# Optimization experiments

Hardware: AMD Instinct MI355X
Metric: run time of the kernel (lower is better)

The kernel has to match this reference:

```python
import jax, jax.numpy as jnp
import numpy as np

SEQ, BATCH, IN_DIM, H1, H2, H3, OUT = 512, 4096, 4, 24, 48, 24, 2


def _rnn_layer(x, W_ih, W_hh, b_ih, b_hh):
    # x: [T, B, in]; torch RNN-relu cell: h_t = relu(x_t W_ih^T + b_ih + h_{t-1} W_hh^T + b_hh)
    pre = jnp.einsum('tbi,hi->tbh', x, W_ih) + (b_ih + b_hh)  # precompute input projection for all t

    def step(h, p):
        h = jax.nn.relu(p + h @ W_hh.T)
        return h, h

    h0 = jnp.zeros((x.shape[1], W_hh.shape[0]), x.dtype)
    _, ys = jax.lax.scan(step, h0, pre)
    return ys  # [T, B, hidden]


def setup_inputs() -> dict:
    key = jax.random.key(0)
    ks = jax.random.split(key, 14)

    def u(k, shape, fan):
        s = 1.0 / np.sqrt(fan)
        return jax.random.uniform(k, shape, jnp.float32, -s, s)

    return {
        'x': jax.random.normal(ks[0], (SEQ, BATCH, IN_DIM), jnp.float32),
        'W_ih0': u(ks[1], (H1, IN_DIM), H1), 'W_hh0': u(ks[2], (H1, H1), H1),
        'b_ih0': u(ks[3], (H1,), H1), 'b_hh0': u(ks[4], (H1,), H1),
        'W_ih1': u(ks[5], (H2, H1), H2), 'W_hh1': u(ks[6], (H2, H2), H2),
        'b_ih1': u(ks[7], (H2,), H2), 'b_hh1': u(ks[8], (H2,), H2),
        'W_ih2': u(ks[9], (H3, H2), H3), 'W_hh2': u(ks[10], (H3, H3), H3),
        'b_ih2': u(ks[11], (H3,), H3), 'b_hh2': u(ks[12], (H3,), H3),
        'W_out': u(ks[13], (OUT, H3), H3),
        'b_out': jnp.zeros((OUT,), jnp.float32),
    }


def reference(x, W_ih0, W_hh0, b_ih0, b_hh0, W_ih1, W_hh1, b_ih1, b_hh1,
              W_ih2, W_hh2, b_ih2, b_hh2, W_out, b_out):
    a1 = _rnn_layer(x, W_ih0, W_hh0, b_ih0, b_hh0)   # [T,B,24]
    a2 = _rnn_layer(a1, W_ih1, W_hh1, b_ih1, b_hh1)  # [T,B,48]
    a3 = _rnn_layer(a2, W_ih2, W_hh2, b_ih2, b_hh2)  # [T,B,24]
    return a3 @ W_out.T + b_out                       # [T,B,2]
```

## Files before the change

kernel.cpp:

```cpp
#include <hip/hip_runtime.h>
#include <hip/hip_fp16.h>


#define TSEQ 512
#define NBAT 4096

typedef float    f32x4 __attribute__((ext_vector_type(4)));
typedef _Float16 f16x8 __attribute__((ext_vector_type(8)));

union BFrag { f16x8 h; unsigned u[4]; };

__device__ __forceinline__ f32x4 MF(f16x8 a, f16x8 b, f32x4 c) {
  return __builtin_amdgcn_mfma_f32_16x16x32_f16(a, b, c, 0, 0, 0);
}
__device__ __forceinline__ unsigned pkh(float a, float b) {
  union { __half2 h2; unsigned u; } x;
  x.h2 = __floats2half2_rn(a, b);
  return x.u;
}
__device__ __forceinline__ unsigned pkr(float a, float b) {
  return pkh(fmaxf(a, 0.f), fmaxf(b, 0.f));
}

#define SBAR __builtin_amdgcn_sched_barrier(0)
#define LGKM_WAIT(n) __builtin_amdgcn_s_waitcnt(0xC07F | ((n) << 8))
#define ENDBAR(R)                                                              \
  do {                                                                         \
    SBAR;                                                                      \
    LGKM_WAIT(R);                                                              \
    __builtin_amdgcn_s_barrier();                                              \
    SBAR;                                                                      \
  } while (0)

#define SW16(PB, U) ((4 * (PB) + (U)) & 15)
#define SR16(PB, U) ((4 * (PB) + (U) + 12) & 15)

struct WP { const float *wih0,*whh0,*wih1,*whh1,*wih2,*whh2,*wout; };

__device__ float wcat(int layer, int m, int k, const WP& P) {
  if (layer == 0) {
    if (m < 24) {
      if (k < 24) return P.whh0[m * 24 + k];
      if (k >= 28 && k < 32) return P.wih0[m * 4 + (k - 28)];
    }
    return 0.f;
  } else if (layer == 1) {
    if (m < 48) {
      if (k < 24) return P.wih1[m * 24 + k];
      if (k >= 32 && k < 80) return P.whh1[m * 48 + (k - 32)];
    }
    return 0.f;
  } else if (layer == 2) {
    if (m < 24) {
      if (k < 48) return P.wih2[m * 48 + k];
      if (k >= 64 && k < 88) return P.whh2[m * 24 + (k - 64)];
    }
    return 0.f;
  } else {
    if (m < 2 && k < 24) return P.wout[m * 24 + k];
    return 0.f;
  }
}

__device__ f16x8 afrag(int layer, int mt, int kc, const WP& P) {
  int m  = mt * 16 + (threadIdx.x & 15);
  int kb = kc * 32 + 4 * ((threadIdx.x >> 4) & 3);
  f16x8 r;
#pragma unroll
  for (int j = 0; j < 4; ++j) r[j] = (_Float16)wcat(layer, m, kb + j, P);
#pragma unroll
  for (int j = 0; j < 4; ++j) r[4 + j] = (_Float16)wcat(layer, m, kb + 16 + j, P);
  return r;
}

__device__ f32x4 cfrag(const float* b1, const float* b2, int mt, int nvalid) {
  int qq = (threadIdx.x >> 4) & 3;
  f32x4 r;
#pragma unroll
  for (int i = 0; i < 4; ++i) {
    int m = mt * 16 + 4 * qq + i;
    float v = 0.f;
    if (m < nvalid) { v = b1[m]; if (b2) v += b2[m]; }
    r[i] = v;
  }
  return r;
}

__global__ void __launch_bounds__(512)
rnn3_p8s4(const float* __restrict__ x,
          const float* __restrict__ wih0, const float* __restrict__ whh0,
          const float* __restrict__ bih0, const float* __restrict__ bhh0,
          const float* __restrict__ wih1, const float* __restrict__ whh1,
          const float* __restrict__ bih1, const float* __restrict__ bhh1,
          const float* __restrict__ wih2, const float* __restrict__ whh2,
          const float* __restrict__ bih2, const float* __restrict__ bhh2,
          const float* __restrict__ wout, const float* __restrict__ bout,
          float* __restrict__ out) {
  __shared__ uint4 sH1[16][64];
  __shared__ f32x4 sP1[16][3][64];
  __shared__ uint4 sH2a[16][64];
  __shared__ uint2 sH2b[16][64];
  __shared__ f32x4 sP2a[16][64];
  __shared__ f32x4 sP2b[16][64];
  __shared__ uint4 sH3[16][64];

  const int tid  = threadIdx.x;
  const int wid  = tid >> 6;
  const int lane = tid & 63;
  const int c = lane & 15;
  const int q = lane >> 4;
  const int b0 = blockIdx.x * 16;

  WP P{wih0, whh0, wih1, whh1, wih2, whh2, wout};
  const float4* x4 = (const float4*)x;
  float2*       o2 = (float2*)out;

  const int NJ = 35;

  if (wid == 0) {
    f16x8 A00 = afrag(0, 0, 0, P), A01 = afrag(0, 1, 0, P);
    f32x4 C00 = cfrag(bih0, bhh0, 0, 24), C01 = cfrag(bih0, bhh0, 1, 24);
    float4 xb[16];
#pragma unroll
    for (int s = 0; s < 16; ++s) xb[s] = x4[(size_t)s * NBAT + b0 + c];
    unsigned fa0 = 0u, fa1 = 0u, fa2 = 0u, fa3 = 0u;

#define A_STEP(PB, U)                                                          \
    {                                                                          \
      float4 xs = xb[SW16(PB, U)];                                             \
      BFrag FAu;                                                               \
      FAu.u[0] = fa0; FAu.u[1] = fa1;                                          \
      FAu.u[2] = (q == 3) ? pkh(xs.x, xs.y) : fa2;                             \
      FAu.u[3] = (q == 3) ? pkh(xs.z, xs.w) : fa3;                             \
      f32x4 a10 = MF(A00, FAu.h, C00);                                         \
      f32x4 a11 = MF(A01, FAu.h, C01);                                         \
      {                                                                        \
        int t = 4 * i + (U);                                                   \
        int tn = (t + 16 < TSEQ) ? t + 16 : TSEQ - 1;                          \
        xb[SW16(PB, U)] = x4[(size_t)tn * NBAT + b0 + c];                      \
      }                                                                        \
      fa0 = pkr(a10[0], a10[1]); fa1 = pkr(a10[2], a10[3]);                    \
      fa2 = pkr(a11[0], a11[1]); fa3 = pkr(a11[2], a11[3]);                    \
      sH1[SW16(PB, U)][lane] = make_uint4(fa0, fa1, fa2, fa3);                 \
    }
#define A_BODY(PB)                                                             \
    {                                                                          \
      int i = i0 + (PB);                                                       \
      if (i <= 127) { A_STEP(PB, 0) A_STEP(PB, 1) A_STEP(PB, 2) A_STEP(PB, 3) }\
      ENDBAR(0);                                                               \
    }
#pragma unroll 1
    for (int J = 0; J < NJ; ++J) {
      int i0 = 4 * J;
      A_BODY(0) A_BODY(1) A_BODY(2) A_BODY(3)
    }
#undef A_BODY
#undef A_STEP

  } else if (wid == 1 || wid == 2) {
    const bool isD = (wid == 1);
    f16x8 W0 = afrag(1, isD ? 0 : 2, 0, P);
    f16x8 W1 = isD ? afrag(1, 1, 0, P) : W0;
    f32x4 Cb0 = cfrag(bih1, bhh1, isD ? 0 : 2, 48);
    f32x4 Cb1 = isD ? cfrag(bih1, bhh1, 1, 48) : Cb0;
    uint4 bufA[4], bufB[4];
#pragma unroll
    for (int s = 0; s < 4; ++s) { bufA[s] = make_uint4(0u,0u,0u,0u); bufB[s] = make_uint4(0u,0u,0u,0u); }

#define D_STEP(PB, U, CUR)                                                     \
    {                                                                          \
      BFrag FAu;                                                               \
      FAu.u[0] = CUR[U].x; FAu.u[1] = CUR[U].y;                                \
      FAu.u[2] = CUR[U].z; FAu.u[3] = CUR[U].w;                                \
      f32x4 p0 = MF(W0, FAu.h, Cb0);                                           \
      if (isD) {                                                               \
        f32x4 p1 = MF(W1, FAu.h, Cb1);                                         \
        sP1[SW16(PB, U)][0][lane] = p0;                                        \
        sP1[SW16(PB, U)][1][lane] = p1;                                        \
      } else {                                                                 \
        sP1[SW16(PB, U)][2][lane] = p0;                                        \
      }                                                                        \
    }
#define D_BODY(PB, CUR, NXT)                                                   \
    {                                                                          \
      int i = i0 + (PB);                                                       \
      if (i >= 2 && i <= 129) {                                                \
        D_STEP(PB, 0, CUR) D_STEP(PB, 1, CUR)                                  \
        D_STEP(PB, 2, CUR) D_STEP(PB, 3, CUR)                                  \
      }                                                                        \
      SBAR;                                                                    \
      NXT[0] = sH1[SR16(PB, 0)][lane];                                         \
      NXT[1] = sH1[SR16(PB, 1)][lane];                                         \
      NXT[2] = sH1[SR16(PB, 2)][lane];                                         \
      NXT[3] = sH1[SR16(PB, 3)][lane];                                         \
      ENDBAR(4);                                                               \
    }
#pragma unroll 1
    for (int J = 0; J < NJ; ++J) {
      int i0 = 4 * J;
      D_BODY(0, bufA, bufB) D_BODY(1, bufB, bufA)
      D_BODY(2, bufA, bufB) D_BODY(3, bufB, bufA)
    }
#undef D_BODY
#undef D_STEP

  } else if (wid == 3) {
    f16x8 A1c1[3], A1c2[3];
#pragma unroll
    for (int mt = 0; mt < 3; ++mt) {
      A1c1[mt] = afrag(1, mt, 1, P);
      A1c2[mt] = afrag(1, mt, 2, P);
    }
    const f32x4 Z4 = {0.f, 0.f, 0.f, 0.f};
    unsigned fb0 = 0u, fb1 = 0u, fb2 = 0u, fb3 = 0u, fc0 = 0u, fc1 = 0u;
    f32x4 pA[4][3], pB[4][3];
#pragma unroll
    for (int s = 0; s < 4; ++s)
#pragma unroll
      for (int m = 0; m < 3; ++m) { pA[s][m] = Z4; pB[s][m] = Z4; }

#define B_STEP(PB, U, CUR)                                                     \
    {                                                                          \
      BFrag FBu, FCu;                                                          \
      FBu.u[0] = fb0; FBu.u[1] = fb1; FBu.u[2] = fb2; FBu.u[3] = fb3;          \
      FCu.u[0] = fc0; FCu.u[1] = fc1; FCu.u[2] = 0u; FCu.u[3] = 0u;            \
      f32x4 aB0 = MF(A1c2[0], FCu.h, Z4);                                      \
      f32x4 aB1 = MF(A1c2[1], FCu.h, Z4);                                      \
      f32x4 aB2 = MF(A1c2[2], FCu.h, Z4);                                      \
      f32x4 aA0 = MF(A1c1[0], FBu.h, CUR[U][0]);                               \
      f32x4 aA1 = MF(A1c1[1], FBu.h, CUR[U][1]);                               \
      f32x4 aA2 = MF(A1c1[2], FBu.h, CUR[U][2]);                               \
      f32x4 s0 = aA0 + aB0, s1 = aA1 + aB1, s2 = aA2 + aB2;                    \
      fb0 = pkr(s0[0], s0[1]); fb1 = pkr(s0[2], s0[3]);                        \
      fb2 = pkr(s1[0], s1[1]); fb3 = pkr(s1[2], s1[3]);                        \
      fc0 = pkr(s2[0], s2[1]); fc1 = pkr(s2[2], s2[3]);                        \
      sH2a[SW16(PB, U)][lane] = make_uint4(fb0, fb1, fb2, fb3);                \
      sH2b[SW16(PB, U)][lane] = make_uint2(fc0, fc1);                          \
    }
#define B_BODY(PB, CUR, NXT)                                                   \
    {                                                                          \
      int i = i0 + (PB);                                                       \
      if (i >= 4 && i <= 131) {                                                \
        B_STEP(PB, 0, CUR) B_STEP(PB, 1, CUR)                                  \
        B_STEP(PB, 2, CUR) B_STEP(PB, 3, CUR)                                  \
      }                                                                        \
      SBAR;                                                                    \
      NXT[0][0] = sP1[SR16(PB, 0)][0][lane];                                   \
      NXT[0][1] = sP1[SR16(PB, 0)][1][lane];                                   \
      NXT[0][2] = sP1[SR16(PB, 0)][2][lane];                                   \
      NXT[1][0] = sP1[SR16(PB, 1)][0][lane];                                   \
      NXT[1][1] = sP1[SR16(PB, 1)][1][lane];                                   \
      NXT[1][2] = sP1[SR16(PB, 1)][2][lane];                                   \
      NXT[2][0] = sP1[SR16(PB, 2)][0][lane];                                   \
      NXT[2][1] = sP1[SR16(PB, 2)][1][lane];                                   \
      NXT[2][2] = sP1[SR16(PB, 2)][2][lane];                                   \
      NXT[3][0] = sP1[SR16(PB, 3)][0][lane];                                   \
      NXT[3][1] = sP1[SR16(PB, 3)][1][lane];                                   \
      NXT[3][2] = sP1[SR16(PB, 3)][2][lane];                                   \
      ENDBAR(12);                                                              \
    }
#pragma unroll 1
    for (int J = 0; J < NJ; ++J) {
      int i0 = 4 * J;
      B_BODY(0, pA, pB) B_BODY(1, pB, pA) B_BODY(2, pA, pB) B_BODY(3, pB, pA)
    }
#undef B_BODY
#undef B_STEP

  } else if (wid == 4 || wid == 5) {
    const int mt = (wid == 4) ? 0 : 1;
    f16x8 W0 = afrag(2, mt, 0, P), W1 = afrag(2, mt, 1, P);
    f32x4 Cb = cfrag(bih2, bhh2, mt, 24);
    uint4 haA[4], haB[4];
    uint2 hbA[4], hbB[4];
#pragma unroll
    for (int s = 0; s < 4; ++s) {
      haA[s] = make_uint4(0u,0u,0u,0u); haB[s] = make_uint4(0u,0u,0u,0u);
      hbA[s] = make_uint2(0u,0u);       hbB[s] = make_uint2(0u,0u);
    }

#define E_STEP(PB, U, CA, CB)                                                  \
    {                                                                          \
      BFrag FBu, FCu;                                                          \
      FBu.u[0] = CA[U].x; FBu.u[1] = CA[U].y;                                  \
      FBu.u[2] = CA[U].z; FBu.u[3] = CA[U].w;                                  \
      FCu.u[0] = CB[U].x; FCu.u[1] = CB[U].y;                                  \
      FCu.u[2] = 0u; FCu.u[3] = 0u;                                            \
      f32x4 p = MF(W0, FBu.h, Cb);                                             \
      p = MF(W1, FCu.h, p);                                                    \
      if (mt == 0) sP2a[SW16(PB, U)][lane] = p;                                \
      else         sP2b[SW16(PB, U)][lane] = p;                                \
    }
#define E_BODY(PB, CA, CB, NA, NB)                                             \
    {                                                                          \
      int i = i0 + (PB);                                                       \
      if (i >= 6 && i <= 133) {                                                \
        E_STEP(PB, 0, CA, CB) E_STEP(PB, 1, CA, CB)                            \
        E_STEP(PB, 2, CA, CB) E_STEP(PB, 3, CA, CB)                            \
      }                                                                        \
      SBAR;                                                                    \
      NA[0] = sH2a[SR16(PB, 0)][lane];                                         \
      NA[1] = sH2a[SR16(PB, 1)][lane];                                         \
      NA[2] = sH2a[SR16(PB, 2)][lane];                                         \
      NA[3] = sH2a[SR16(PB, 3)][lane];                                         \
      NB[0] = sH2b[SR16(PB, 0)][lane];                                         \
      NB[1] = sH2b[SR16(PB, 1)][lane];                                         \
      NB[2] = sH2b[SR16(PB, 2)][lane];                                         \
      NB[3] = sH2b[SR16(PB, 3)][lane];                                         \
      ENDBAR(8);                                                               \
    }
#pragma unroll 1
    for (int J = 0; J < NJ; ++J) {
      int i0 = 4 * J;
      E_BODY(0, haA, hbA, haB, hbB) E_BODY(1, haB, hbB, haA, hbA)
      E_BODY(2, haA, hbA, haB, hbB) E_BODY(3, haB, hbB, haA, hbA)
    }
#undef E_BODY
#undef E_STEP

  } else if (wid == 6) {
    f16x8 A2c2m0 = afrag(2, 0, 2, P), A2c2m1 = afrag(2, 1, 2, P);
    unsigned fd0 = 0u, fd1 = 0u, fd2 = 0u, fd3 = 0u;
    const f32x4 Z4 = {0.f, 0.f, 0.f, 0.f};
    f32x4 paA[4], paB[4], pbA[4], pbB[4];
#pragma unroll
    for (int s = 0; s < 4; ++s) { paA[s] = Z4; paB[s] = Z4; pbA[s] = Z4; pbB[s] = Z4; }

#define C_STEP(PB, U, CA, CB)                                                  \
    {                                                                          \
      BFrag FDu;                                                               \
      FDu.u[0] = fd0; FDu.u[1] = fd1; FDu.u[2] = fd2; FDu.u[3] = fd3;          \
      f32x4 a30 = MF(A2c2m0, FDu.h, CA[U]);                                    \
      f32x4 a31 = MF(A2c2m1, FDu.h, CB[U]);                                    \
      fd0 = pkr(a30[0], a30[1]); fd1 = pkr(a30[2], a30[3]);                    \
      fd2 = pkr(a31[0], a31[1]); fd3 = pkr(a31[2], a31[3]);                    \
      sH3[SW16(PB, U)][lane] = make_uint4(fd0, fd1, fd2, fd3);                 \
    }
#define C_BODY(PB, CA, CB, NA, NB)                                             \
    {                                                                          \
      int i = i0 + (PB);                                                       \
      if (i >= 8 && i <= 135) {                                                \
        C_STEP(PB, 0, CA, CB) C_STEP(PB, 1, CA, CB)                            \
        C_STEP(PB, 2, CA, CB) C_STEP(PB, 3, CA, CB)                            \
      }                                                                        \
      SBAR;                                                                    \
      NA[0] = sP2a[SR16(PB, 0)][lane];                                         \
      NA[1] = sP2a[SR16(PB, 1)][lane];                                         \
      NA[2] = sP2a[SR16(PB, 2)][lane];                                         \
      NA[3] = sP2a[SR16(PB, 3)][lane];                                         \
      NB[0] = sP2b[SR16(PB, 0)][lane];                                         \
      NB[1] = sP2b[SR16(PB, 1)][lane];                                         \
      NB[2] = sP2b[SR16(PB, 2)][lane];                                         \
      NB[3] = sP2b[SR16(PB, 3)][lane];                                         \
      ENDBAR(8);                                                               \
    }
#pragma unroll 1
    for (int J = 0; J < NJ; ++J) {
      int i0 = 4 * J;
      C_BODY(0, paA, pbA, paB, pbB) C_BODY(1, paB, pbB, paA, pbA)
      C_BODY(2, paA, pbA, paB, pbB) C_BODY(3, paB, pbB, paA, pbA)
    }
#undef C_BODY
#undef C_STEP

  } else {
    f16x8 A3 = afrag(3, 0, 0, P);
    f32x4 C3 = cfrag(bout, nullptr, 0, 2);
    uint4 h3A[4], h3B[4];
#pragma unroll
    for (int s = 0; s < 4; ++s) { h3A[s] = make_uint4(0u,0u,0u,0u); h3B[s] = make_uint4(0u,0u,0u,0u); }

#define G_STEP(PB, U, CUR)                                                     \
    {                                                                          \
      BFrag FDu;                                                               \
      FDu.u[0] = CUR[U].x; FDu.u[1] = CUR[U].y;                                \
      FDu.u[2] = CUR[U].z; FDu.u[3] = CUR[U].w;                                \
      f32x4 ao = MF(A3, FDu.h, C3);                                            \
      int t = 4 * i - 40 + (U);                                                \
      if (q == 0)                                                              \
        o2[(size_t)t * NBAT + b0 + c] = make_float2(ao[0], ao[1]);             \
    }
#define G_BODY(PB, CUR, NXT)                                                   \
    {                                                                          \
      int i = i0 + (PB);                                                       \
      if (i >= 10 && i <= 137) {                                               \
        G_STEP(PB, 0, CUR) G_STEP(PB, 1, CUR)                                  \
        G_STEP(PB, 2, CUR) G_STEP(PB, 3, CUR)                                  \
      }                                                                        \
      SBAR;                                                                    \
      NXT[0] = sH3[SR16(PB, 0)][lane];                                         \
      NXT[1] = sH3[SR16(PB, 1)][lane];                                         \
      NXT[2] = sH3[SR16(PB, 2)][lane];                                         \
      NXT[3] = sH3[SR16(PB, 3)][lane];                                         \
      ENDBAR(4);                                                               \
    }
#pragma unroll 1
    for (int J = 0; J < NJ; ++J) {
      int i0 = 4 * J;
      G_BODY(0, h3A, h3B) G_BODY(1, h3B, h3A)
      G_BODY(2, h3A, h3B) G_BODY(3, h3B, h3A)
    }
#undef G_BODY
#undef G_STEP
  }
}

extern "C" void kernel_launch(void* const* d_in, const int* in_sizes, int n_in,
                              void* d_out, int out_size, void* d_ws, size_t ws_size,
                              hipStream_t stream) {
  const float* x    = (const float*)d_in[0];
  const float* wih0 = (const float*)d_in[1];
  const float* whh0 = (const float*)d_in[2];
  const float* bih0 = (const float*)d_in[3];
  const float* bhh0 = (const float*)d_in[4];
  const float* wih1 = (const float*)d_in[5];
  const float* whh1 = (const float*)d_in[6];
  const float* bih1 = (const float*)d_in[7];
  const float* bhh1 = (const float*)d_in[8];
  const float* wih2 = (const float*)d_in[9];
  const float* whh2 = (const float*)d_in[10];
  const float* bih2 = (const float*)d_in[11];
  const float* bhh2 = (const float*)d_in[12];
  const float* wout = (const float*)d_in[13];
  const float* bout = (const float*)d_in[14];
  float* out = (float*)d_out;

  rnn3_p8s4<<<dim3(NBAT / 16), dim3(512), 0, stream>>>(
      x, wih0, whh0, bih0, bhh0, wih1, whh1, bih1, bhh1,
      wih2, whh2, bih2, bhh2, wout, bout, out);
}
```

Measured before the change: 84.74 us.

## Fuse output projection into layer-3 warp and make last warp a store-only stage

The output linear layer (W_out MFMA) moves from the final warp into the warp that computes layer 3, which now writes the small float2 results to a new shared buffer instead of the full h3 fragments. The final warp only reads these and stores them to global memory. This shrinks shared-memory traffic for h3 and takes one pipeline stage's MFMA off the last warp, at the cost of an extra MFMA on the layer-3 critical path. The step windows shift by one iteration to match. The layer-1 B-step MFMA order is also swapped so the accumulate-dependent MFMAs issue first.

```diff
diff --git a/kernel.cpp b/kernel.cpp
--- a/kernel.cpp
+++ b/kernel.cpp
@@ -32,8 +32,10 @@
     SBAR;                                                                      \
   } while (0)
 
-#define SW16(PB, U) ((4 * (PB) + (U)) & 15)
-#define SR16(PB, U) ((4 * (PB) + (U) + 12) & 15)
+#define SW16(PB, U)  ((4 * (PB) + (U)) & 15)
+#define SR16(PB, U)  ((4 * (PB) + (U) + 12) & 15)
+#define SWAO(PB, U)  ((4 * (PB) + (U) + 15) & 15)
+#define SRAO(PB, U)  ((4 * (PB) + (U) + 11) & 15)
 
 struct WP { const float *wih0,*whh0,*wih1,*whh1,*wih2,*whh2,*wout; };
 
@@ -87,22 +89,22 @@
 }
 
 __global__ void __launch_bounds__(512)
-rnn3_p8s4(const float* __restrict__ x,
-          const float* __restrict__ wih0, const float* __restrict__ whh0,
-          const float* __restrict__ bih0, const float* __restrict__ bhh0,
-          const float* __restrict__ wih1, const float* __restrict__ whh1,
-          const float* __restrict__ bih1, const float* __restrict__ bhh1,
-          const float* __restrict__ wih2, const float* __restrict__ whh2,
-          const float* __restrict__ bih2, const float* __restrict__ bhh2,
-          const float* __restrict__ wout, const float* __restrict__ bout,
-          float* __restrict__ out) {
-  __shared__ uint4 sH1[16][64];
-  __shared__ f32x4 sP1[16][3][64];
-  __shared__ uint4 sH2a[16][64];
-  __shared__ uint2 sH2b[16][64];
-  __shared__ f32x4 sP2a[16][64];
-  __shared__ f32x4 sP2b[16][64];
-  __shared__ uint4 sH3[16][64];
+rnn3_p8r12(const float* __restrict__ x,
+           const float* __restrict__ wih0, const float* __restrict__ whh0,
+           const float* __restrict__ bih0, const float* __restrict__ bhh0,
+           const float* __restrict__ wih1, const float* __restrict__ whh1,
+           const float* __restrict__ bih1, const float* __restrict__ bhh1,
+           const float* __restrict__ wih2, const float* __restrict__ whh2,
+           const float* __restrict__ bih2, const float* __restrict__ bhh2,
+           const float* __restrict__ wout, const float* __restrict__ bout,
+           float* __restrict__ out) {
+  __shared__ uint4  sH1[16][64];
+  __shared__ f32x4  sP1[16][3][64];
+  __shared__ uint4  sH2a[16][64];
+  __shared__ uint2  sH2b[16][64];
+  __shared__ f32x4  sP2a[16][64];
+  __shared__ f32x4  sP2b[16][64];
+  __shared__ float2 sAO[16][16];
 
   const int tid  = threadIdx.x;
   const int wid  = tid >> 6;
@@ -224,12 +226,12 @@
       BFrag FBu, FCu;                                                          \
       FBu.u[0] = fb0; FBu.u[1] = fb1; FBu.u[2] = fb2; FBu.u[3] = fb3;          \
       FCu.u[0] = fc0; FCu.u[1] = fc1; FCu.u[2] = 0u; FCu.u[3] = 0u;            \
+      f32x4 aA0 = MF(A1c1[0], FBu.h, CUR[U][0]);                               \
+      f32x4 aA1 = MF(A1c1[1], FBu.h, CUR[U][1]);                               \
+      f32x4 aA2 = MF(A1c1[2], FBu.h, CUR[U][2]);                               \
       f32x4 aB0 = MF(A1c2[0], FCu.h, Z4);                                      \
       f32x4 aB1 = MF(A1c2[1], FCu.h, Z4);                                      \
       f32x4 aB2 = MF(A1c2[2], FCu.h, Z4);                                      \
-      f32x4 aA0 = MF(A1c1[0], FBu.h, CUR[U][0]);                               \
-      f32x4 aA1 = MF(A1c1[1], FBu.h, CUR[U][1]);                               \
-      f32x4 aA2 = MF(A1c1[2], FBu.h, CUR[U][2]);                               \
       f32x4 s0 = aA0 + aB0, s1 = aA1 + aB1, s2 = aA2 + aB2;                    \
       fb0 = pkr(s0[0], s0[1]); fb1 = pkr(s0[2], s0[3]);                        \
       fb2 = pkr(s1[0], s1[1]); fb3 = pkr(s1[2], s1[3]);                        \
@@ -320,6 +322,8 @@
 
   } else if (wid == 6) {
     f16x8 A2c2m0 = afrag(2, 0, 2, P), A2c2m1 = afrag(2, 1, 2, P);
+    f16x8 A3 = afrag(3, 0, 0, P);
+    f32x4 C3 = cfrag(bout, nullptr, 0, 2);
     unsigned fd0 = 0u, fd1 = 0u, fd2 = 0u, fd3 = 0u;
     const f32x4 Z4 = {0.f, 0.f, 0.f, 0.f};
     f32x4 paA[4], paB[4], pbA[4], pbB[4];
@@ -330,16 +334,19 @@
     {                                                                          \
       BFrag FDu;                                                               \
       FDu.u[0] = fd0; FDu.u[1] = fd1; FDu.u[2] = fd2; FDu.u[3] = fd3;          \
+      f32x4 ao = MF(A3, FDu.h, C3);                           \
       f32x4 a30 = MF(A2c2m0, FDu.h, CA[U]);                                    \
       f32x4 a31 = MF(A2c2m1, FDu.h, CB[U]);                                    \
+      int th = 4 * i - 33 + (U);                                               \
+      if (th >= 0 && th < TSEQ && q == 0)                                      \
+        sAO[SWAO(PB, U)][c] = make_float2(ao[0], ao[1]);                       \
       fd0 = pkr(a30[0], a30[1]); fd1 = pkr(a30[2], a30[3]);                    \
       fd2 = pkr(a31[0], a31[1]); fd3 = pkr(a31[2], a31[3]);                    \
-      sH3[SW16(PB, U)][lane] = make_uint4(fd0, fd1, fd2, fd3);                 \
     }
 #define C_BODY(PB, CA, CB, NA, NB)                                             \
     {                                                                          \
       int i = i0 + (PB);                                                       \
-      if (i >= 8 && i <= 135) {                                                \
+      if (i >= 8 && i <= 136) {                                                \
         C_STEP(PB, 0, CA, CB) C_STEP(PB, 1, CA, CB)                            \
         C_STEP(PB, 2, CA, CB) C_STEP(PB, 3, CA, CB)                            \
       }                                                                        \
@@ -364,44 +371,38 @@
 #undef C_STEP
 
   } else {
-    f16x8 A3 = afrag(3, 0, 0, P);
-    f32x4 C3 = cfrag(bout, nullptr, 0, 2);
-    uint4 h3A[4], h3B[4];
-#pragma unroll
-    for (int s = 0; s < 4; ++s) { h3A[s] = make_uint4(0u,0u,0u,0u); h3B[s] = make_uint4(0u,0u,0u,0u); }
-
-#define G_STEP(PB, U, CUR)                                                     \
-    {                                                                          \
-      BFrag FDu;                                                               \
-      FDu.u[0] = CUR[U].x; FDu.u[1] = CUR[U].y;                                \
-      FDu.u[2] = CUR[U].z; FDu.u[3] = CUR[U].w;                                \
-      f32x4 ao = MF(A3, FDu.h, C3);                                            \
-      int t = 4 * i - 40 + (U);                                                \
-      if (q == 0)                                                              \
-        o2[(size_t)t * NBAT + b0 + c] = make_float2(ao[0], ao[1]);             \
-    }
-#define G_BODY(PB, CUR, NXT)                                                   \
-    {                                                                          \
-      int i = i0 + (PB);                                                       \
-      if (i >= 10 && i <= 137) {                                               \
-        G_STEP(PB, 0, CUR) G_STEP(PB, 1, CUR)                                  \
-        G_STEP(PB, 2, CUR) G_STEP(PB, 3, CUR)                                  \
+    float2 aoA[4], aoB[4];
+#pragma unroll
+    for (int s = 0; s < 4; ++s) { aoA[s] = make_float2(0.f, 0.f); aoB[s] = make_float2(0.f, 0.f); }
+
+#define S_STEP(PB, U, CUR)                                                     \
+    {                                                                          \
+      int t = 4 * i - 41 + (U);                                                \
+      if (t >= 0 && t < TSEQ && q == 0)                                        \
+        o2[(size_t)t * NBAT + b0 + c] = CUR[U];                                \
+    }
+#define S_BODY(PB, CUR, NXT)                                                   \
+    {                                                                          \
+      int i = i0 + (PB);                                                       \
+      if (i >= 10 && i <= 138) {                                               \
+        S_STEP(PB, 0, CUR) S_STEP(PB, 1, CUR)                                  \
+        S_STEP(PB, 2, CUR) S_STEP(PB, 3, CUR)                                  \
       }                                                                        \
       SBAR;                                                                    \
-      NXT[0] = sH3[SR16(PB, 0)][lane];                                         \
-      NXT[1] = sH3[SR16(PB, 1)][lane];                                         \
-      NXT[2] = sH3[SR16(PB, 2)][lane];                                         \
-      NXT[3] = sH3[SR16(PB, 3)][lane];                                         \
+      NXT[0] = sAO[SRAO(PB, 0)][c];                                            \
+      NXT[1] = sAO[SRAO(PB, 1)][c];                                            \
+      NXT[2] = sAO[SRAO(PB, 2)][c];                                            \
+      NXT[3] = sAO[SRAO(PB, 3)][c];                                            \
       ENDBAR(4);                                                               \
     }
 #pragma unroll 1
     for (int J = 0; J < NJ; ++J) {
       int i0 = 4 * J;
-      G_BODY(0, h3A, h3B) G_BODY(1, h3B, h3A)
-      G_BODY(2, h3A, h3B) G_BODY(3, h3B, h3A)
-    }
-#undef G_BODY
-#undef G_STEP
+      S_BODY(0, aoA, aoB) S_BODY(1, aoB, aoA)
+      S_BODY(2, aoA, aoB) S_BODY(3, aoB, aoA)
+    }
+#undef S_BODY
+#undef S_STEP
   }
 }
 
@@ -425,7 +426,7 @@
   const float* bout = (const float*)d_in[14];
   float* out = (float*)d_out;
 
-  rnn3_p8s4<<<dim3(NBAT / 16), dim3(512), 0, stream>>>(
+  rnn3_p8r12<<<dim3(NBAT / 16), dim3(512), 0, stream>>>(
       x, wih0, whh0, bih0, bhh0, wih1, whh1, bih1, bhh1,
       wih2, whh2, bih2, bhh2, wout, bout, out);
 }
```

After: 84.91 us. Within noise of the previous version (+0.2%).
